# Optimization experiments

Measured on AMD Instinct MI355X. Metric: run time of the kernel, lower is better.

The kernel has to match this reference:

```python
import jax, jax.numpy as jnp
import numpy as np

N_NODES = 50000
N_EDGES = 800000
NUM_RELS = 16
IN_DIM = 16      # == NUM_RELS (one-hot of op_class_id)
H_DIM = 128
OUT_DIM = 128    # must equal H_DIM (actor/critic consume output-layer root feats)
LIN_DIM = 512


def setup_inputs() -> dict:
    key = jax.random.key(0)
    ks = jax.random.split(key, 16)
    op_class_id = jax.random.randint(ks[0], (N_NODES,), 0, NUM_RELS, dtype=jnp.int32)
    norm = jax.random.uniform(ks[1], (N_NODES,), dtype=jnp.float32)
    src = jax.random.randint(ks[2], (N_EDGES,), 0, N_NODES, dtype=jnp.int32)
    dst = jax.random.randint(ks[3], (N_EDGES,), 0, N_NODES, dtype=jnp.int32)
    s = 0.1
    W0 = jax.random.normal(ks[4], (NUM_RELS, IN_DIM, H_DIM), jnp.float32) * s
    W1 = jax.random.normal(ks[5], (NUM_RELS, H_DIM, H_DIM), jnp.float32) * s
    W2 = jax.random.normal(ks[6], (NUM_RELS, H_DIM, OUT_DIM), jnp.float32) * s
    a1_w = jax.random.normal(ks[7], (OUT_DIM, LIN_DIM), jnp.float32) * s
    a1_b = jnp.zeros((LIN_DIM,), jnp.float32)
    a2_w = jax.random.normal(ks[8], (LIN_DIM, OUT_DIM), jnp.float32) * s
    a2_b = jnp.zeros((OUT_DIM,), jnp.float32)
    c1_w = jax.random.normal(ks[9], (OUT_DIM, LIN_DIM), jnp.float32) * s
    c1_b = jnp.zeros((LIN_DIM,), jnp.float32)
    c2_w = jax.random.normal(ks[10], (LIN_DIM, 1), jnp.float32) * s
    c2_b = jnp.zeros((1,), jnp.float32)
    return dict(op_class_id=op_class_id, norm=norm, src=src, dst=dst,
                W0=W0, W1=W1, W2=W2,
                a1_w=a1_w, a1_b=a1_b, a2_w=a2_w, a2_b=a2_b,
                c1_w=c1_w, c1_b=c1_b, c2_w=c2_w, c2_b=c2_b)


def _rgcn_layer(h, cls, norm, src, dst, W, act):
    # per-node relation-specific transform: h[n] @ W[cls[n]]
    # compute all relations then select (R small, avoids [N,in,out] gather)
    stacked = jnp.einsum('ni,rio->rno', h, W)          # [R, N, out]
    msg = stacked[cls, jnp.arange(h.shape[0])]         # [N, out]
    msg = msg * norm[:, None]
    agg = jax.ops.segment_sum(msg[src], dst, num_segments=h.shape[0])
    return act(agg)


def reference(op_class_id, norm, src, dst, W0, W1, W2,
              a1_w, a1_b, a2_w, a2_b, c1_w, c1_b, c2_w, c2_b):
    one_hot = jax.nn.one_hot(op_class_id, IN_DIM, dtype=jnp.float32)  # op_class_one_hot
    h = _rgcn_layer(one_hot, op_class_id, norm, src, dst, W0, jax.nn.relu)
    h = _rgcn_layer(h, op_class_id, norm, src, dst, W1, jax.nn.relu)
    h = _rgcn_layer(h, op_class_id, norm, src, dst, W2,
                    lambda x: jax.nn.softmax(x, axis=1))
    root = h[0]                                        # [OUT_DIM]
    probs = jax.nn.relu(root @ a1_w + a1_b) @ a2_w + a2_b
    value = jax.nn.relu(root @ c1_w + c1_b) @ c2_w + c2_b
    return probs, value
```

## Files before the change

### kernel.cpp

```cpp
#include <hip/hip_runtime.h>

#define NN 50000
#define NE 800000
#define NQ (NE / 4)
#define NR 16
#define HD 128
#define LIND 512

#define E0CAP 4096
#define SEGN 16
#define SEGCAP 2048

#define PZ ((int)0xAAAAAAAA)

#define CNT(i) cnt[(i) * 16]
#define L_E0      0
#define L_E1(s)   (1 + (s))
#define L_SCAN(s) (17 + (s))
#define L_EDGE(s) (33 + (s))
#define L_DONE    49

#define NEB 256
#define NTB (NEB + NR + 16)

__global__ void k_scanA(const int* __restrict__ src, const int* __restrict__ dst,
                        int* map1, int* e0_src, int* cnt) {
    int tid = blockIdx.x * blockDim.x + threadIdx.x;
    if (tid >= NQ) return;
    int4 d4 = ((const int4*)dst)[tid];
    int ds[4] = {d4.x, d4.y, d4.z, d4.w};
    #pragma unroll
    for (int j = 0; j < 4; j++) {
        if (ds[j] == 0) {
            int s = src[4 * tid + j];
            int i = atomicAdd(&CNT(L_E0), 1) - PZ;
            if (i >= 0 && i < E0CAP) e0_src[i] = s;
            map1[s] = 1;
        }
    }
}

__global__ void k_scanB1(const int* __restrict__ src, const int* __restrict__ dst,
                         const int* __restrict__ cls, const float* __restrict__ norm,
                         const int* __restrict__ map1, int* map0,
                         int4* e1seg, int* cnt) {
    int tid = blockIdx.x * blockDim.x + threadIdx.x;
    if (tid >= NQ) return;
    int seg = blockIdx.x & (SEGN - 1);
    int4 d4 = ((const int4*)dst)[tid];
    int ds[4] = {d4.x, d4.y, d4.z, d4.w};
    #pragma unroll
    for (int j = 0; j < 4; j++) {
        if (map1[ds[j]] == 1) {
            int s = src[4 * tid + j];
            int i = atomicAdd(&CNT(L_E1(seg)), 1) - PZ;
            if (i >= 0 && i < SEGCAP)
                e1seg[seg * SEGCAP + i] =
                    make_int4(s, ds[j], cls[s], __float_as_int(norm[s]));
            map0[s] = 1;
        }
    }
}

__global__ void __launch_bounds__(256, 2)
k_tail5(const int* __restrict__ src, const int* __restrict__ dst,
        const int* __restrict__ cls, const float* __restrict__ norm,
        const int* __restrict__ map0, int* cnt,
        const int* __restrict__ e0_src, const int4* __restrict__ e1seg,
        float* w0sum, float* agg1, float* rootpre,
        const float* __restrict__ W0, const float* __restrict__ W1,
        const float* __restrict__ W2,
        const float* __restrict__ a1w, const float* __restrict__ a1b,
        const float* __restrict__ a2w, const float* __restrict__ a2b,
        const float* __restrict__ c1w, const float* __restrict__ c1b,
        const float* __restrict__ c2w, const float* __restrict__ c2b,
        float* out) {
    const int t = threadIdx.x;
    const int b = blockIdx.x;

    __shared__ union {
        struct { float shw[NR]; float sha[HD]; float red[256]; } ed;
        struct { float u[HD]; int si[256]; int sc[256]; float sn[256]; int any; } rt;
        struct { float sha[HD]; float shz[64]; float red[256]; } mlp;
    } sm;

    {
        const int4* d4p = (const int4*)dst;
        for (int q = b * 256 + t; q < NQ; q += NTB * 256) {
            int4 d4 = d4p[q];
            int ds[4] = {d4.x, d4.y, d4.z, d4.w};
            #pragma unroll
            for (int j = 0; j < 4; j++) {
                if (map0[ds[j]] == 1) {
                    int s = src[4 * q + j];
                    atomicAdd(&w0sum[((size_t)ds[j] << 4) + cls[s]], norm[s]);
                }
            }
        }
    }
    __syncthreads();
    if (t == 0)
        __hip_atomic_fetch_add(&CNT(L_SCAN(b & (SEGN - 1))), 1,
                               __ATOMIC_RELAXED, __HIP_MEMORY_SCOPE_AGENT);

    if (b < NEB) {
        const int seg = b & (SEGN - 1);
        const int own = b >> 4;
        int len = CNT(L_E1(seg)) - PZ;
        if (len < 0) len = 0; if (len > SEGCAP) len = SEGCAP;
        const int o = t & 127, hf = t >> 7, kk0 = hf << 6;
        int u = 0, v = 0, c = 0; float nm = 0.f;
        float w1reg[64];
        float w0reg[NR];
        if (t < HD) {
            #pragma unroll
            for (int cc = 0; cc < NR; cc++) w0reg[cc] = W0[cc * 2176 + t];
        }
        bool have = (own < len);
        if (have) {
            int4 e = e1seg[seg * SEGCAP + own];
            u = e.x; v = e.y; c = e.z; nm = __int_as_float(e.w);
            const float* w = W1 + c * (HD * HD) + o;
            #pragma unroll
            for (int k = 0; k < 64; k++) w1reg[k] = w[(kk0 + k) << 7];
        }
        if (t == 0) {
            for (;;) {
                int tot = 0;
                #pragma unroll
                for (int s2 = 0; s2 < SEGN; s2++)
                    tot += __hip_atomic_load(&CNT(L_SCAN(s2)), __ATOMIC_RELAXED,
                                             __HIP_MEMORY_SCOPE_AGENT) - PZ;
                if (tot >= NTB) break;
                __builtin_amdgcn_s_sleep(1);
            }
        }
        __syncthreads();
        for (int i = own; i < len; i += NEB / SEGN) {
            if (i != own) {
                int4 e = e1seg[seg * SEGCAP + i];
                u = e.x; v = e.y; c = e.z; nm = __int_as_float(e.w);
                const float* w = W1 + c * (HD * HD) + o;
                #pragma unroll
                for (int k = 0; k < 64; k++) w1reg[k] = w[(kk0 + k) << 7];
            }
            if (t < NR)
                sm.ed.shw[t] = __hip_atomic_load(&w0sum[((size_t)u << 4) + t],
                                                 __ATOMIC_RELAXED,
                                                 __HIP_MEMORY_SCOPE_AGENT);
            __syncthreads();
            if (t < HD) {
                float a = 0.f;
                #pragma unroll
                for (int cc = 0; cc < NR; cc++) a = fmaf(sm.ed.shw[cc], w0reg[cc], a);
                sm.ed.sha[t] = fmaxf(a, 0.f);
            }
            __syncthreads();
            {
                float acc = 0.f;
                #pragma unroll
                for (int k = 0; k < 64; k++)
                    acc = fmaf(sm.ed.sha[kk0 + k], w1reg[k], acc);
                sm.ed.red[t] = acc;
            }
            __syncthreads();
            if (t < HD)
                atomicAdd(&agg1[((size_t)v << 7) + t],
                          (sm.ed.red[t] + sm.ed.red[t + 128]) * nm);
            __syncthreads();
        }
        __syncthreads();
        if (t == 0)
            __hip_atomic_fetch_add(&CNT(L_EDGE(seg)), 1,
                                   __ATOMIC_RELAXED, __HIP_MEMORY_SCOPE_AGENT);
    } else if (b < NEB + NR) {
        const int c = b - NEB;
        const int o = t & 127, hf = t >> 7, kk0 = hf << 6;
        if (t < HD) sm.rt.u[t] = 0.f;
        if (t == 0) sm.rt.any = 0;
        int e0n = CNT(L_E0) - PZ;
        if (e0n < 0) e0n = 0; if (e0n > E0CAP) e0n = E0CAP;
        if (t < e0n && t < 256) {
            int s0 = e0_src[t];
            sm.rt.si[t] = s0; sm.rt.sc[t] = cls[s0]; sm.rt.sn[t] = norm[s0];
        }
        float w2reg[64];
        {
            const float* w2 = W2 + c * (HD * HD) + o;
            #pragma unroll
            for (int k = 0; k < 64; k++) w2reg[k] = w2[(kk0 + k) << 7];
        }
        __syncthreads();
        if (t == 0) {
            for (;;) {
                int tot = 0;
                #pragma unroll
                for (int s2 = 0; s2 < SEGN; s2++)
                    tot += __hip_atomic_load(&CNT(L_EDGE(s2)), __ATOMIC_RELAXED,
                                             __HIP_MEMORY_SCOPE_AGENT) - PZ;
                if (tot >= NEB) break;
                __builtin_amdgcn_s_sleep(1);
            }
        }
        __syncthreads();
        for (int base = 0; base < e0n; base += 256) {
            int nchunk = e0n - base; if (nchunk > 256) nchunk = 256;
            if (base > 0) {
                if (t < nchunk) {
                    int s0 = e0_src[base + t];
                    sm.rt.si[t] = s0; sm.rt.sc[t] = cls[s0]; sm.rt.sn[t] = norm[s0];
                }
                __syncthreads();
            }
            for (int i = 0; i < nchunk; i++) {
                if (sm.rt.sc[i] != c) continue;
                if (t < HD) {
                    float av = __hip_atomic_load(&agg1[((size_t)sm.rt.si[i] << 7) + t],
                                                 __ATOMIC_RELAXED,
                                                 __HIP_MEMORY_SCOPE_AGENT);
                    sm.rt.u[t] += sm.rt.sn[i] * fmaxf(av, 0.f);
                }
                if (t == 0) sm.rt.any = 1;
            }
            __syncthreads();
        }
        if (sm.rt.any) {
            float acc = 0.f;
            #pragma unroll
            for (int k = 0; k < 64; k++) acc = fmaf(sm.rt.u[kk0 + k], w2reg[k], acc);
            atomicAdd(&rootpre[o], acc);
        }
        __syncthreads();
        if (t == 0)
            __hip_atomic_fetch_add(&CNT(L_DONE), 1,
                                   __ATOMIC_RELEASE, __HIP_MEMORY_SCOPE_AGENT);
    } else {
        const int bb = b - NEB - NR;
        const int m = bb >> 3, g = bb & 7, k0 = g << 6;
        const float* Wh = m ? c1w : a1w;
        const float* bh = m ? c1b : a1b;
        const int o1 = t & 63, qu = t >> 6, kk1 = qu << 5;
        float wreg[32];
        #pragma unroll
        for (int i = 0; i < 32; i++) wreg[i] = Wh[(kk1 + i) * LIND + k0 + o1];
        float breg = bh[k0 + o1];
        const int o2 = t & 127, hf2 = t >> 7, j2 = hf2 << 5;
        float vreg[32];
        if (m == 0) {
            #pragma unroll
            for (int j = 0; j < 32; j++) vreg[j] = a2w[(k0 + j2 + j) * HD + o2];
        } else {
            vreg[0] = c2w[k0 + o1];
        }
        if (t == 0) {
            while (__hip_atomic_load(&CNT(L_DONE), __ATOMIC_ACQUIRE,
                                     __HIP_MEMORY_SCOPE_AGENT) - PZ < NR)
                __builtin_amdgcn_s_sleep(2);
        }
        __syncthreads();
        if (t < HD)
            sm.mlp.sha[t] = __hip_atomic_load(&rootpre[t], __ATOMIC_RELAXED,
                                              __HIP_MEMORY_SCOPE_AGENT);
        __syncthreads();
        float mx = -3.0e38f;
        for (int i = 0; i < HD; i++) mx = fmaxf(mx, sm.mlp.sha[i]);
        float ex = (t < HD) ? expf(sm.mlp.sha[t] - mx) : 0.f;
        __syncthreads();
        if (t < HD) sm.mlp.sha[t] = ex;
        __syncthreads();
        float sum = 0.f;
        for (int i = 0; i < HD; i++) sum += sm.mlp.sha[i];
        __syncthreads();
        if (t < HD) sm.mlp.sha[t] = ex / sum;
        __syncthreads();
        {
            float z = 0.f;
            #pragma unroll
            for (int i = 0; i < 32; i++) z = fmaf(sm.mlp.sha[kk1 + i], wreg[i], z);
            sm.mlp.red[t] = z;
            __syncthreads();
            if (t < 64)
                sm.mlp.shz[t] = fmaxf(breg + sm.mlp.red[t] + sm.mlp.red[t + 64]
                                      + sm.mlp.red[t + 128] + sm.mlp.red[t + 192], 0.f);
        }
        __syncthreads();
        if (m == 0) {
            float acc = 0.f;
            #pragma unroll
            for (int j = 0; j < 32; j++) acc = fmaf(sm.mlp.shz[j2 + j], vreg[j], acc);
            sm.mlp.red[t] = acc;
            __syncthreads();
            if (t < HD) {
                float v = sm.mlp.red[t] + sm.mlp.red[t + 128];
                if (bb == 0) v += a2b[t];
                atomicAdd(&out[t], v);
            }
        } else {
            if (t < 64) sm.mlp.red[t] = sm.mlp.shz[t] * vreg[0];
            __syncthreads();
            if (t == 0) {
                float v = (bb == 8) ? c2b[0] : 0.f;
                for (int j = 0; j < 64; j++) v += sm.mlp.red[j];
                atomicAdd(&out[HD], v);
            }
        }
    }
}

extern "C" void kernel_launch(void* const* d_in, const int* in_sizes, int n_in,
                              void* d_out, int out_size, void* d_ws, size_t ws_size,
                              hipStream_t stream) {
    const int*   cls  = (const int*)d_in[0];
    const float* norm = (const float*)d_in[1];
    const int*   src  = (const int*)d_in[2];
    const int*   dst  = (const int*)d_in[3];
    const float* W0   = (const float*)d_in[4];
    const float* W1   = (const float*)d_in[5];
    const float* W2   = (const float*)d_in[6];
    const float* a1w  = (const float*)d_in[7];
    const float* a1b  = (const float*)d_in[8];
    const float* a2w  = (const float*)d_in[9];
    const float* a2b  = (const float*)d_in[10];
    const float* c1w  = (const float*)d_in[11];
    const float* c1b  = (const float*)d_in[12];
    const float* c2w  = (const float*)d_in[13];
    const float* c2b  = (const float*)d_in[14];
    float* out = (float*)d_out;

    char*  ws      = (char*)d_ws;
    int*   cnt     = (int*)(ws + 0);
    int*   e0_src  = (int*)(ws + 4096);
    float* rootpre = (float*)(ws + 20480);
    int4*  e1seg   = (int4*)(ws + 32768);
    int*   map1    = (int*)(ws + 589824);
    int*   map0    = (int*)(ws + 819200);
    float* w0sum   = (float*)(ws + 1048576);
    float* agg1    = (float*)(ws + 8388608);

    k_scanA<<<1024, 256, 0, stream>>>(src, dst, map1, e0_src, cnt);
    k_scanB1<<<1024, 256, 0, stream>>>(src, dst, cls, norm, map1, map0, e1seg, cnt);
    k_tail5<<<NTB, 256, 0, stream>>>(src, dst, cls, norm, map0, cnt, e0_src, e1seg,
                                     w0sum, agg1, rootpre, W0, W1, W2,
                                     a1w, a1b, a2w, a2b, c1w, c1b, c2w, c2b, out);
}
```

Before: 117.9 us.

## Replace node maps with shared-memory bitmap and small-list membership test

The dense int map0 becomes a 1600-word bitmap that k_scanA clears with its spare threads. k_scanB1 sets bits in it with atomicOr, and k_tail6 copies it into shared memory so the membership test on dst no longer does random global loads. k_scanB1 also tests dst against a shared list of the layer-0 source nodes when there are at most 64 of them, instead of reading map1 from global memory. The cost is atomicOr contention on bitmap words, an extra shared-memory staging step, and a linear scan per edge in the small-list path.

```diff
diff --git a/kernel.cpp b/kernel.cpp
--- a/kernel.cpp
+++ b/kernel.cpp
@@ -10,6 +10,8 @@
 #define E0CAP 4096
 #define SEGN 16
 #define SEGCAP 2048
+#define S1MAX 64
+#define BMW 1600
 
 #define PZ ((int)0xAAAAAAAA)
 
@@ -24,9 +26,13 @@
 #define NTB (NEB + NR + 16)
 
 __global__ void k_scanA(const int* __restrict__ src, const int* __restrict__ dst,
-                        int* map1, int* e0_src, int* cnt) {
+                        int* map1, int* e0_src, int* cnt, int* map0bm) {
     int tid = blockIdx.x * blockDim.x + threadIdx.x;
-    if (tid >= NQ) return;
+    if (tid >= NQ) {
+        int idx = tid - NQ;
+        if (idx < BMW) map0bm[idx] = 0;
+        return;
+    }
     int4 d4 = ((const int4*)dst)[tid];
     int ds[4] = {d4.x, d4.y, d4.z, d4.w};
     #pragma unroll
@@ -42,8 +48,14 @@
 
 __global__ void k_scanB1(const int* __restrict__ src, const int* __restrict__ dst,
                          const int* __restrict__ cls, const float* __restrict__ norm,
-                         const int* __restrict__ map1, int* map0,
-                         int4* e1seg, int* cnt) {
+                         const int* __restrict__ map1, const int* __restrict__ e0_src,
+                         int* map0bm, int4* e1seg, int* cnt) {
+    __shared__ int s1l[S1MAX];
+    int e0n = CNT(L_E0) - PZ;
+    if (e0n < 0) e0n = 0; if (e0n > E0CAP) e0n = E0CAP;
+    const int s1n = (e0n <= S1MAX) ? e0n : 0;
+    if (threadIdx.x < s1n) s1l[threadIdx.x] = e0_src[threadIdx.x];
+    __syncthreads();
     int tid = blockIdx.x * blockDim.x + threadIdx.x;
     if (tid >= NQ) return;
     int seg = blockIdx.x & (SEGN - 1);
@@ -51,21 +63,29 @@
     int ds[4] = {d4.x, d4.y, d4.z, d4.w};
     #pragma unroll
     for (int j = 0; j < 4; j++) {
-        if (map1[ds[j]] == 1) {
+        int dv = ds[j];
+        bool hit;
+        if (s1n) {
+            hit = false;
+            for (int s2 = 0; s2 < s1n; s2++) hit |= (dv == s1l[s2]);
+        } else {
+            hit = (map1[dv] == 1);
+        }
+        if (hit) {
             int s = src[4 * tid + j];
             int i = atomicAdd(&CNT(L_E1(seg)), 1) - PZ;
             if (i >= 0 && i < SEGCAP)
                 e1seg[seg * SEGCAP + i] =
-                    make_int4(s, ds[j], cls[s], __float_as_int(norm[s]));
-            map0[s] = 1;
+                    make_int4(s, dv, cls[s], __float_as_int(norm[s]));
+            atomicOr(&map0bm[s >> 5], 1 << (s & 31));
         }
     }
 }
 
 __global__ void __launch_bounds__(256, 2)
-k_tail5(const int* __restrict__ src, const int* __restrict__ dst,
+k_tail6(const int* __restrict__ src, const int* __restrict__ dst,
         const int* __restrict__ cls, const float* __restrict__ norm,
-        const int* __restrict__ map0, int* cnt,
+        const int* __restrict__ map0bm, int* cnt,
         const int* __restrict__ e0_src, const int4* __restrict__ e1seg,
         float* w0sum, float* agg1, float* rootpre,
         const float* __restrict__ W0, const float* __restrict__ W1,
@@ -79,21 +99,25 @@
     const int b = blockIdx.x;
 
     __shared__ union {
+        int bm[BMW];
         struct { float shw[NR]; float sha[HD]; float red[256]; } ed;
         struct { float u[HD]; int si[256]; int sc[256]; float sn[256]; int any; } rt;
         struct { float sha[HD]; float shz[64]; float red[256]; } mlp;
     } sm;
 
     {
+        for (int i = t; i < BMW; i += 256) sm.bm[i] = map0bm[i];
+        __syncthreads();
         const int4* d4p = (const int4*)dst;
         for (int q = b * 256 + t; q < NQ; q += NTB * 256) {
             int4 d4 = d4p[q];
             int ds[4] = {d4.x, d4.y, d4.z, d4.w};
             #pragma unroll
             for (int j = 0; j < 4; j++) {
-                if (map0[ds[j]] == 1) {
+                int dv = ds[j];
+                if ((sm.bm[dv >> 5] >> (dv & 31)) & 1) {
                     int s = src[4 * q + j];
-                    atomicAdd(&w0sum[((size_t)ds[j] << 4) + cls[s]], norm[s]);
+                    atomicAdd(&w0sum[((size_t)dv << 4) + cls[s]], norm[s]);
                 }
             }
         }
@@ -331,15 +355,16 @@
     int*   cnt     = (int*)(ws + 0);
     int*   e0_src  = (int*)(ws + 4096);
     float* rootpre = (float*)(ws + 20480);
+    int*   map0bm  = (int*)(ws + 24576);
     int4*  e1seg   = (int4*)(ws + 32768);
     int*   map1    = (int*)(ws + 589824);
-    int*   map0    = (int*)(ws + 819200);
     float* w0sum   = (float*)(ws + 1048576);
     float* agg1    = (float*)(ws + 8388608);
 
-    k_scanA<<<1024, 256, 0, stream>>>(src, dst, map1, e0_src, cnt);
-    k_scanB1<<<1024, 256, 0, stream>>>(src, dst, cls, norm, map1, map0, e1seg, cnt);
-    k_tail5<<<NTB, 256, 0, stream>>>(src, dst, cls, norm, map0, cnt, e0_src, e1seg,
+    k_scanA<<<1024, 256, 0, stream>>>(src, dst, map1, e0_src, cnt, map0bm);
+    k_scanB1<<<1024, 256, 0, stream>>>(src, dst, cls, norm, map1, e0_src,
+                                       map0bm, e1seg, cnt);
+    k_tail6<<<NTB, 256, 0, stream>>>(src, dst, cls, norm, map0bm, cnt, e0_src, e1seg,
                                      w0sum, agg1, rootpre, W0, W1, W2,
                                      a1w, a1b, a2w, a2b, c1w, c1b, c2w, c2b, out);
 }
```

New measurement: 115.3 us. 2.3% less time.
